# Optimization experiments

Hardware: AMD Instinct MI355X
Metric: run time of the kernel (lower is better)

Reference implementation:

```python
import jax, jax.numpy as jnp
import numpy as np

MUL = 1024
DIMS = [3, 5, 7, 9]          # irrep dims for l=1,2,3,4
BN_EPS = 1e-5                # e3nn BatchNorm eps
ACT_EPS = 1e-8               # numerical guard for norm-activation sqrt
INV_SQRT_MUL = 1.0 / np.sqrt(MUL)


def bn_act(f, w):
    """e3nn BatchNorm (training mode, component normalization, mean reduce)
    followed by NormActivation(sigmoid, normalize=True).
    f: [B, mul, d] one irrep block; w: [mul] affine batchnorm weight."""
    # norm-based batchnorm: second moment per multiplicity channel
    var = jnp.mean(jnp.mean(f * f, axis=-1), axis=0)            # [mul]
    f = f * ((var + BN_EPS) ** -0.5 * w)[None, :, None]
    # norm-gated sigmoid: out = f * sigmoid(||f||) / ||f||
    n = jnp.sqrt(jnp.sum(f * f, axis=-1, keepdims=True) + ACT_EPS)  # [B, mul, 1]
    return f * (jax.nn.sigmoid(n) / n)


def setup_inputs() -> dict:
    key = jax.random.key(0)
    k = jax.random.split(key, 4)
    B = 1024
    x = jax.random.normal(k[0], (B, 2, 3, 1), dtype=jnp.float32)
    w1 = jax.random.normal(k[1], (2, MUL), dtype=jnp.float32)
    W = jax.random.normal(k[2], (5, 4, MUL, MUL), dtype=jnp.float32)
    bn_w = jnp.ones((6, 4, MUL), dtype=jnp.float32)
    w_out = jax.random.normal(k[3], (MUL, 1), dtype=jnp.float32)
    return {"x": x, "w1": w1, "W": W, "bn_w": bn_w, "w_out": w_out}


def reference(x, w1, W, bn_w, w_out):
    B = x.shape[0]
    x = x.reshape(B, 2, 3)  # '2x1e'
    # block1: only the l=1 path exists; l=2,3,4 outputs are zero
    f1 = jnp.einsum('bui,uv->bvi', x, w1) * (1.0 / jnp.sqrt(2.0).astype(x.dtype))
    fields = [bn_act(f1, bn_w[0, 0])]
    for i, d in enumerate(DIMS[1:]):
        fields.append(bn_act(jnp.zeros((B, MUL, d), x.dtype), bn_w[0, i + 1]))
    # blocks 2..6: per-irrep block linear + norm batchnorm + norm activation
    for b in range(5):
        fields = [
            bn_act(jnp.einsum('bui,uv->bvi', f, W[b, i]) * INV_SQRT_MUL,
                   bn_w[b + 1, i])
            for i, f in enumerate(fields)
        ]
    # out linear: '1024x1e' -> '1x1e'
    out = jnp.einsum('bui,uv->bvi', fields[0], w_out) * INV_SQRT_MUL  # [B,1,3]
    return out.reshape(B, 3)
```

## Files before the change

### kernel.cpp

```cpp
#include <hip/hip_runtime.h>
#include <hip/hip_bf16.h>
#include <cstdint>
#include <cstddef>


typedef short    s16x8 __attribute__((ext_vector_type(8)));
typedef float    f32x4 __attribute__((ext_vector_type(4)));

#define PLANE 1048576

__device__ __forceinline__ unsigned short f2bf(float f) {
  unsigned u = __builtin_bit_cast(unsigned, f);
  u += 0x7FFFu + ((u >> 16) & 1u);
  return (unsigned short)(u >> 16);
}
__device__ __forceinline__ float bf2f(unsigned short h) {
  return __builtin_bit_cast(float, (unsigned)h << 16);
}

__device__ __forceinline__ size_t ablk(int row, int k) {
  return ((size_t)(row >> 6) << 17) + ((size_t)(k >> 5) << 12)
       + ((size_t)((row >> 4) & 3) << 10) + ((size_t)((k >> 3) & 3) << 8)
       + ((size_t)(row & 15) << 4) + ((size_t)(k & 7) << 1);
}

__device__ __forceinline__ void load_lds16(const void* g, void* l) {
  __builtin_amdgcn_global_load_lds(
      (const __attribute__((address_space(1))) unsigned int*)g,
      (__attribute__((address_space(3))) unsigned int*)l,
      16, 0, 0);
}

__global__ void convert_w(const float* __restrict__ W,
                          unsigned short* __restrict__ Wh,
                          unsigned short* __restrict__ Wl) {
  __shared__ float t[64][65];
  const int u0 = blockIdx.x * 64, v0 = blockIdx.y * 64;
  const float* Wb = W + (size_t)blockIdx.z * 4194304;
  char* Whb = (char*)(Wh + (size_t)blockIdx.z * PLANE);
  char* Wlb = (char*)(Wl + (size_t)blockIdx.z * PLANE);
  const int c = threadIdx.x & 63, r4 = threadIdx.x >> 6;
#pragma unroll
  for (int i = 0; i < 16; ++i) {
    const int r = i * 4 + r4;
    t[r][c] = Wb[(size_t)(u0 + r) * 1024 + v0 + c];
  }
  __syncthreads();
#pragma unroll
  for (int i = 0; i < 16; ++i) {
    const int r = i * 4 + r4;
    const float w = t[c][r] * 0.03125f;
    const unsigned short hi = f2bf(w);
    const size_t off = ablk(v0 + r, u0 + c);
    *(unsigned short*)(Whb + off) = hi;
    *(unsigned short*)(Wlb + off) = f2bf(w - bf2f(hi));
  }
}

__global__ void layer0_fused(const float* __restrict__ x, const float* __restrict__ w1,
                             float* __restrict__ pre, float* __restrict__ var) {
  const int v = blockIdx.x * 256 + threadIdx.x;
  const int b0 = blockIdx.y * 16;
  const float a0 = w1[v], a1 = w1[1024 + v];
  const float inv = 0.70710678118654752f;
  float ssq = 0.f;
#pragma unroll 4
  for (int bb = 0; bb < 16; ++bb) {
    const int b = b0 + bb;
    const float* xb = x + b * 6;
#pragma unroll
    for (int i = 0; i < 3; ++i) {
      const float f = (xb[i] * a0 + xb[3 + i] * a1) * inv;
      pre[(size_t)i * PLANE + (size_t)b * 1024 + v] = f;
      ssq += f * f;
    }
  }
  atomicAdd(&var[v], ssq);
}

__global__ void act_kernel(const float* __restrict__ pre, const float* __restrict__ var,
                           const float* __restrict__ bnw,
                           char* __restrict__ ah, char* __restrict__ al) {
  const int tid = threadIdx.x;
  const int b  = blockIdx.x * 16 + (tid & 15);
  const int v0 = blockIdx.y * 128 + (tid >> 4) * 8;
  float s[8];
#pragma unroll
  for (int j = 0; j < 8; ++j)
    s[j] = bnw[v0 + j] / sqrtf(var[v0 + j] * (1.0f / 3072.0f) + 1e-5f);
  float f[3][8];
#pragma unroll
  for (int i = 0; i < 3; ++i) {
    const float4 p0 = *(const float4*)&pre[(size_t)i * PLANE + (size_t)b * 1024 + v0];
    const float4 p1 = *(const float4*)&pre[(size_t)i * PLANE + (size_t)b * 1024 + v0 + 4];
    f[i][0] = p0.x * s[0]; f[i][1] = p0.y * s[1]; f[i][2] = p0.z * s[2]; f[i][3] = p0.w * s[3];
    f[i][4] = p1.x * s[4]; f[i][5] = p1.y * s[5]; f[i][6] = p1.z * s[6]; f[i][7] = p1.w * s[7];
  }
#pragma unroll
  for (int j = 0; j < 8; ++j) {
    const float n = sqrtf(f[0][j] * f[0][j] + f[1][j] * f[1][j] + f[2][j] * f[2][j] + 1e-8f);
    const float g = 1.0f / ((1.0f + expf(-n)) * n);
    f[0][j] *= g; f[1][j] *= g; f[2][j] *= g;
  }
#pragma unroll
  for (int i = 0; i < 3; ++i) {
    s16x8 hi, lo;
#pragma unroll
    for (int j = 0; j < 8; ++j) {
      const unsigned short h = f2bf(f[i][j]);
      hi[j] = (short)h;
      lo[j] = (short)f2bf(f[i][j] - bf2f(h));
    }
    const size_t off = ablk(i * 1024 + b, v0);
    *(s16x8*)(ah + off) = hi;
    *(s16x8*)(al + off) = lo;
  }
}

__global__ __launch_bounds__(256, 3) void gemm_fused(
    const char* __restrict__ Ah, const char* __restrict__ Al,
    const char* __restrict__ Bh, const char* __restrict__ Bl,
    float* __restrict__ C, float* __restrict__ var) {
  __shared__ unsigned short lds[3][4][4][4][16][8];
  const int tid = threadIdx.x;
  const int bid = blockIdx.x;
  const int xcd = bid & 7, q = bid >> 3;
  const int bm0 = (xcd * 6 + (q % 6)) * 64;
  const int bn0 = (q / 6) * 64;
  const int lane = tid & 63, wave = tid >> 6;
  const int wm = (wave >> 1) * 32, wn = (wave & 1) * 32;
  const int rsel = lane & 15, kcsel = lane >> 4;

  f32x4 acc[2][2] = {};

  const size_t abase = ((size_t)(bm0 >> 6) << 17) + (wave << 10) + (lane << 4);
  const size_t bbase = ((size_t)(bn0 >> 6) << 17) + (wave << 10) + (lane << 4);
  const char* g0 = Ah + abase;
  const char* g1 = Al + abase;
  const char* g2 = Bh + bbase;
  const char* g3 = Bl + bbase;

  auto stage = [&](int buf, int t) {
    const size_t kb = (size_t)t << 12;
    char* base = (char*)lds + buf * 16384 + (wave << 10);
    load_lds16(g0 + kb, base);
    load_lds16(g1 + kb, base + 4096);
    load_lds16(g2 + kb, base + 8192);
    load_lds16(g3 + kb, base + 12288);
  };

  const int fo = kcsel * 256 + rsel * 16;
  auto compute = [&](int buf) {
    const char* p = (const char*)lds + buf * 16384;
    s16x8 fah[2], fal[2], fbh[2], fbl[2];
#pragma unroll
    for (int m = 0; m < 2; ++m) {
      fah[m] = *(const s16x8*)(p         + ((wm >> 4) + m) * 1024 + fo);
      fal[m] = *(const s16x8*)(p + 4096  + ((wm >> 4) + m) * 1024 + fo);
    }
#pragma unroll
    for (int n = 0; n < 2; ++n) {
      fbh[n] = *(const s16x8*)(p + 8192  + ((wn >> 4) + n) * 1024 + fo);
      fbl[n] = *(const s16x8*)(p + 12288 + ((wn >> 4) + n) * 1024 + fo);
    }
#pragma unroll
    for (int m = 0; m < 2; ++m)
#pragma unroll
      for (int n = 0; n < 2; ++n) {
        acc[m][n] = __builtin_amdgcn_mfma_f32_16x16x32_bf16(fal[m], fbh[n], acc[m][n], 0, 0, 0);
        acc[m][n] = __builtin_amdgcn_mfma_f32_16x16x32_bf16(fah[m], fbl[n], acc[m][n], 0, 0, 0);
        acc[m][n] = __builtin_amdgcn_mfma_f32_16x16x32_bf16(fah[m], fbh[n], acc[m][n], 0, 0, 0);
      }
  };

  stage(0, 0);
  stage(1, 1);
  int cb = 0, sb = 2;
  for (int t = 0; t < 30; ++t) {
    stage(sb, t + 2);
    __builtin_amdgcn_sched_barrier(0);
    asm volatile("s_waitcnt vmcnt(8)" ::: "memory");
    __builtin_amdgcn_sched_barrier(0);
    __builtin_amdgcn_s_barrier();
    compute(cb);
    __builtin_amdgcn_sched_barrier(0);
    __builtin_amdgcn_s_barrier();
    sb = cb;
    cb = (cb == 2) ? 0 : cb + 1;
  }
  asm volatile("s_waitcnt vmcnt(4)" ::: "memory");
  __builtin_amdgcn_sched_barrier(0);
  __builtin_amdgcn_s_barrier();
  compute(0);
  asm volatile("s_waitcnt vmcnt(0)" ::: "memory");
  __builtin_amdgcn_sched_barrier(0);
  __builtin_amdgcn_s_barrier();
  compute(1);

  const int r0 = bm0 + wm + (kcsel << 2);
  const int c0 = bn0 + wn + rsel;
  float csq[2] = {0.f, 0.f};
#pragma unroll
  for (int m = 0; m < 2; ++m)
#pragma unroll
    for (int n = 0; n < 2; ++n)
#pragma unroll
      for (int j = 0; j < 4; ++j) {
        const float v = acc[m][n][j];
        C[(size_t)(r0 + m * 16 + j) * 1024 + c0 + n * 16] = v;
        csq[n] += v * v;
      }
#pragma unroll
  for (int n = 0; n < 2; ++n) {
    csq[n] += __shfl_xor(csq[n], 16);
    csq[n] += __shfl_xor(csq[n], 32);
  }
  if (kcsel == 0) {
#pragma unroll
    for (int n = 0; n < 2; ++n)
      atomicAdd(&var[c0 + n * 16], csq[n]);
  }
}

__global__ void final_kernel(const char* __restrict__ ah, const char* __restrict__ al,
                             const float* __restrict__ wout, float* __restrict__ out) {
  const int b = blockIdx.x, tid = threadIdx.x;
  __shared__ float red[3][4];
  float s[3] = {0.f, 0.f, 0.f};
  if (tid < 128) {
    const int v0 = tid * 8;
#pragma unroll
    for (int i = 0; i < 3; ++i) {
      const size_t off = ablk(i * 1024 + b, v0);
      const s16x8 hi = *(const s16x8*)(ah + off);
      const s16x8 lo = *(const s16x8*)(al + off);
#pragma unroll
      for (int j = 0; j < 8; ++j)
        s[i] += (bf2f((unsigned short)hi[j]) + bf2f((unsigned short)lo[j])) * wout[v0 + j];
    }
  }
#pragma unroll
  for (int i = 0; i < 3; ++i)
    for (int o = 32; o >= 1; o >>= 1) s[i] += __shfl_down(s[i], o);
  if ((tid & 63) == 0)
#pragma unroll
    for (int i = 0; i < 3; ++i) red[i][tid >> 6] = s[i];
  __syncthreads();
  if (tid < 3) {
    const float t = red[tid][0] + red[tid][1] + red[tid][2] + red[tid][3];
    out[b * 3 + tid] = t * 0.03125f;
  }
}

extern "C" void kernel_launch(void* const* d_in, const int* in_sizes, int n_in,
                              void* d_out, int out_size, void* d_ws, size_t ws_size,
                              hipStream_t stream) {
  const float* x    = (const float*)d_in[0];
  const float* w1   = (const float*)d_in[1];
  const float* W    = (const float*)d_in[2];
  const float* bnw  = (const float*)d_in[3];
  const float* wout = (const float*)d_in[4];
  float* out = (float*)d_out;

  char* ws = (char*)d_ws;
  float*          var = (float*)ws;
  float*          pre = (float*)(ws + 32768);
  char*           ah  = ws + 12615680;
  char*           al  = ws + 18907136;
  unsigned short* wh  = (unsigned short*)(ws + 25198592);
  unsigned short* wl  = (unsigned short*)(ws + 35684352);

  hipMemsetAsync(var, 0, 6 * 1024 * sizeof(float), stream);
  convert_w<<<dim3(16, 16, 5), 256, 0, stream>>>(W, wh, wl);
  layer0_fused<<<dim3(4, 64), 256, 0, stream>>>(x, w1, pre, var);
  act_kernel<<<dim3(64, 8), 256, 0, stream>>>(pre, var, bnw, ah, al);
  for (int b = 0; b < 5; ++b) {
    gemm_fused<<<768, 256, 0, stream>>>(
        ah, al, (const char*)(wh + (size_t)b * PLANE), (const char*)(wl + (size_t)b * PLANE),
        pre, var + (b + 1) * 1024);
    act_kernel<<<dim3(64, 8), 256, 0, stream>>>(pre, var + (b + 1) * 1024,
                                                bnw + (size_t)(b + 1) * 4096, ah, al);
  }
  final_kernel<<<1024, 256, 0, stream>>>(ah, al, wout, out);
}
```

Measured before the change: 207.6 us.

## Enlarge GEMM tiles to 128x128 with 512 threads and blocked C layout

The GEMM block tile grows from 64x64 with 256 threads to 128x128 with 512 threads and 8 waves, each wave computing 64x32. Pipelining drops from triple to double LDS buffering, and the grid shrinks from 768 to 192 blocks. C is written in a wave-blocked layout so each store is lane-contiguous, and the activation kernel reads it back through a matching index function. The aim is more operand reuse per LDS load and more coalesced C stores, at the cost of 192 blocks on a 256-CU part (under one wave of blocks), lower occupancy and shallower prefetch.

```diff
diff --git a/kernel.cpp b/kernel.cpp
--- a/kernel.cpp
+++ b/kernel.cpp
@@ -22,6 +22,17 @@
   return ((size_t)(row >> 6) << 17) + ((size_t)(k >> 5) << 12)
        + ((size_t)((row >> 4) & 3) << 10) + ((size_t)((k >> 3) & 3) << 8)
        + ((size_t)(row & 15) << 4) + ((size_t)(k & 7) << 1);
+}
+
+__device__ __forceinline__ size_t cblk(int r, int c) {
+  const int tM = r >> 7, tN = c >> 7;
+  const int rr = r & 127, cc = c & 127;
+  const int wave = ((rr >> 6) << 2) | (cc >> 5);
+  const int m = (rr >> 4) & 3, j = rr & 3;
+  const int n = (cc >> 4) & 1;
+  const int lane = (((rr >> 2) & 3) << 4) | (cc & 15);
+  return (((size_t)((tM * 8 + tN) * 8 + wave)) << 11)
+       + (size_t)(((((m << 1) | n) << 2) | j) << 6) + lane;
 }
 
 __device__ __forceinline__ void load_lds16(const void* g, void* l) {
@@ -78,7 +89,8 @@
   atomicAdd(&var[v], ssq);
 }
 
-__global__ void act_kernel(const float* __restrict__ pre, const float* __restrict__ var,
+template <bool BLK>
+__global__ void act_kernel(const float* __restrict__ Cin, const float* __restrict__ var,
                            const float* __restrict__ bnw,
                            char* __restrict__ ah, char* __restrict__ al) {
   const int tid = threadIdx.x;
@@ -91,8 +103,15 @@
   float f[3][8];
 #pragma unroll
   for (int i = 0; i < 3; ++i) {
-    const float4 p0 = *(const float4*)&pre[(size_t)i * PLANE + (size_t)b * 1024 + v0];
-    const float4 p1 = *(const float4*)&pre[(size_t)i * PLANE + (size_t)b * 1024 + v0 + 4];
+    float4 p0, p1;
+    if (BLK) {
+      const size_t ci = cblk(i * 1024 + b, v0);
+      p0 = *(const float4*)&Cin[ci];
+      p1 = *(const float4*)&Cin[ci + 4];
+    } else {
+      p0 = *(const float4*)&Cin[(size_t)i * PLANE + (size_t)b * 1024 + v0];
+      p1 = *(const float4*)&Cin[(size_t)i * PLANE + (size_t)b * 1024 + v0 + 4];
+    }
     f[i][0] = p0.x * s[0]; f[i][1] = p0.y * s[1]; f[i][2] = p0.z * s[2]; f[i][3] = p0.w * s[3];
     f[i][4] = p1.x * s[4]; f[i][5] = p1.y * s[5]; f[i][6] = p1.z * s[6]; f[i][7] = p1.w * s[7];
   }
@@ -117,54 +136,55 @@
   }
 }
 
-__global__ __launch_bounds__(256, 3) void gemm_fused(
+__global__ __launch_bounds__(512, 2) void gemm_fused(
     const char* __restrict__ Ah, const char* __restrict__ Al,
     const char* __restrict__ Bh, const char* __restrict__ Bl,
     float* __restrict__ C, float* __restrict__ var) {
-  __shared__ unsigned short lds[3][4][4][4][16][8];
+  __shared__ unsigned short lds[2][32][4][16][8];
   const int tid = threadIdx.x;
   const int bid = blockIdx.x;
   const int xcd = bid & 7, q = bid >> 3;
-  const int bm0 = (xcd * 6 + (q % 6)) * 64;
-  const int bn0 = (q / 6) * 64;
+  const int bm0 = (xcd * 3 + (q % 3)) * 128;
+  const int bn0 = (q / 3) * 128;
   const int lane = tid & 63, wave = tid >> 6;
-  const int wm = (wave >> 1) * 32, wn = (wave & 1) * 32;
+  const int wr = wave >> 2, wc = wave & 3;
   const int rsel = lane & 15, kcsel = lane >> 4;
 
-  f32x4 acc[2][2] = {};
-
-  const size_t abase = ((size_t)(bm0 >> 6) << 17) + (wave << 10) + (lane << 4);
-  const size_t bbase = ((size_t)(bn0 >> 6) << 17) + (wave << 10) + (lane << 4);
-  const char* g0 = Ah + abase;
-  const char* g1 = Al + abase;
-  const char* g2 = Bh + bbase;
-  const char* g3 = Bl + bbase;
+  f32x4 acc[4][2] = {};
+
+  const char* gsrc[4];
+#pragma unroll
+  for (int l = 0; l < 4; ++l) {
+    const int g = wave * 4 + l;
+    const int mat = g >> 3, rb = (g >> 2) & 1, wq = g & 3;
+    const char* base = (mat == 0) ? Ah : (mat == 1) ? Al : (mat == 2) ? Bh : Bl;
+    const int rowblk = ((mat < 2) ? (bm0 >> 6) : (bn0 >> 6)) + rb;
+    gsrc[l] = base + ((size_t)rowblk << 17) + (wq << 10) + (lane << 4);
+  }
 
   auto stage = [&](int buf, int t) {
-    const size_t kb = (size_t)t << 12;
-    char* base = (char*)lds + buf * 16384 + (wave << 10);
-    load_lds16(g0 + kb, base);
-    load_lds16(g1 + kb, base + 4096);
-    load_lds16(g2 + kb, base + 8192);
-    load_lds16(g3 + kb, base + 12288);
+    char* ld = (char*)lds + (buf << 15) + wave * 4096;
+#pragma unroll
+    for (int l = 0; l < 4; ++l)
+      load_lds16(gsrc[l] + ((size_t)t << 12), ld + l * 1024);
   };
 
   const int fo = kcsel * 256 + rsel * 16;
   auto compute = [&](int buf) {
-    const char* p = (const char*)lds + buf * 16384;
-    s16x8 fah[2], fal[2], fbh[2], fbl[2];
-#pragma unroll
-    for (int m = 0; m < 2; ++m) {
-      fah[m] = *(const s16x8*)(p         + ((wm >> 4) + m) * 1024 + fo);
-      fal[m] = *(const s16x8*)(p + 4096  + ((wm >> 4) + m) * 1024 + fo);
+    const char* p = (const char*)lds + (buf << 15);
+    s16x8 fah[4], fal[4], fbh[2], fbl[2];
+#pragma unroll
+    for (int m = 0; m < 4; ++m) {
+      fah[m] = *(const s16x8*)(p + ((wr * 4 + m) << 10) + fo);
+      fal[m] = *(const s16x8*)(p + ((8 + wr * 4 + m) << 10) + fo);
     }
 #pragma unroll
     for (int n = 0; n < 2; ++n) {
-      fbh[n] = *(const s16x8*)(p + 8192  + ((wn >> 4) + n) * 1024 + fo);
-      fbl[n] = *(const s16x8*)(p + 12288 + ((wn >> 4) + n) * 1024 + fo);
-    }
-#pragma unroll
-    for (int m = 0; m < 2; ++m)
+      fbh[n] = *(const s16x8*)(p + ((16 + wc * 2 + n) << 10) + fo);
+      fbl[n] = *(const s16x8*)(p + ((24 + wc * 2 + n) << 10) + fo);
+    }
+#pragma unroll
+    for (int m = 0; m < 4; ++m)
 #pragma unroll
       for (int n = 0; n < 2; ++n) {
         acc[m][n] = __builtin_amdgcn_mfma_f32_16x16x32_bf16(fal[m], fbh[n], acc[m][n], 0, 0, 0);
@@ -174,40 +194,33 @@
   };
 
   stage(0, 0);
-  stage(1, 1);
-  int cb = 0, sb = 2;
-  for (int t = 0; t < 30; ++t) {
-    stage(sb, t + 2);
+  for (int t = 0; t < 31; ++t) {
+    stage((t + 1) & 1, t + 1);
     __builtin_amdgcn_sched_barrier(0);
-    asm volatile("s_waitcnt vmcnt(8)" ::: "memory");
+    asm volatile("s_waitcnt vmcnt(4)" ::: "memory");
     __builtin_amdgcn_sched_barrier(0);
     __builtin_amdgcn_s_barrier();
-    compute(cb);
+    compute(t & 1);
     __builtin_amdgcn_sched_barrier(0);
     __builtin_amdgcn_s_barrier();
-    sb = cb;
-    cb = (cb == 2) ? 0 : cb + 1;
-  }
-  asm volatile("s_waitcnt vmcnt(4)" ::: "memory");
+  }
   __builtin_amdgcn_sched_barrier(0);
-  __builtin_amdgcn_s_barrier();
-  compute(0);
   asm volatile("s_waitcnt vmcnt(0)" ::: "memory");
   __builtin_amdgcn_sched_barrier(0);
   __builtin_amdgcn_s_barrier();
   compute(1);
 
-  const int r0 = bm0 + wm + (kcsel << 2);
-  const int c0 = bn0 + wn + rsel;
+  const int tM = bm0 >> 7, tN = bn0 >> 7;
+  float* cw = C + (((size_t)((tM * 8 + tN) * 8 + wave)) << 11) + lane;
   float csq[2] = {0.f, 0.f};
 #pragma unroll
-  for (int m = 0; m < 2; ++m)
+  for (int m = 0; m < 4; ++m)
 #pragma unroll
     for (int n = 0; n < 2; ++n)
 #pragma unroll
       for (int j = 0; j < 4; ++j) {
         const float v = acc[m][n][j];
-        C[(size_t)(r0 + m * 16 + j) * 1024 + c0 + n * 16] = v;
+        cw[((((m << 1) | n) << 2) | j) << 6] = v;
         csq[n] += v * v;
       }
 #pragma unroll
@@ -218,7 +231,7 @@
   if (kcsel == 0) {
 #pragma unroll
     for (int n = 0; n < 2; ++n)
-      atomicAdd(&var[c0 + n * 16], csq[n]);
+      atomicAdd(&var[bn0 + wc * 32 + n * 16 + rsel], csq[n]);
   }
 }
 
@@ -273,13 +286,13 @@
   hipMemsetAsync(var, 0, 6 * 1024 * sizeof(float), stream);
   convert_w<<<dim3(16, 16, 5), 256, 0, stream>>>(W, wh, wl);
   layer0_fused<<<dim3(4, 64), 256, 0, stream>>>(x, w1, pre, var);
-  act_kernel<<<dim3(64, 8), 256, 0, stream>>>(pre, var, bnw, ah, al);
+  act_kernel<false><<<dim3(64, 8), 256, 0, stream>>>(pre, var, bnw, ah, al);
   for (int b = 0; b < 5; ++b) {
-    gemm_fused<<<768, 256, 0, stream>>>(
+    gemm_fused<<<192, 512, 0, stream>>>(
         ah, al, (const char*)(wh + (size_t)b * PLANE), (const char*)(wl + (size_t)b * PLANE),
         pre, var + (b + 1) * 1024);
-    act_kernel<<<dim3(64, 8), 256, 0, stream>>>(pre, var + (b + 1) * 1024,
-                                                bnw + (size_t)(b + 1) * 4096, ah, al);
+    act_kernel<true><<<dim3(64, 8), 256, 0, stream>>>(pre, var + (b + 1) * 1024,
+                                                      bnw + (size_t)(b + 1) * 4096, ah, al);
   }
   final_kernel<<<1024, 256, 0, stream>>>(ah, al, wout, out);
 }
```

New measurement: 220.1 us. 6.0% more time.

## Replace LDS-staged 4-wave GEMM with single-wave register double-buffered GEMM

Applied to the files above, without the earlier changes.

The 64x64 output tile per block is now computed by one wave that loads A/B fragments directly from global memory into registers, double-buffered across k-steps. This drops the LDS staging and the block barriers. Each wave now holds a 4x4 accumulator tile and issues 48 MFMAs per k-step. The cost is four times fewer waves per block, higher register pressure, and no explicit wait control, so memory latency must be hidden by the register prefetch and by occupancy.

```diff
diff --git a/kernel.cpp b/kernel.cpp
--- a/kernel.cpp
+++ b/kernel.cpp
@@ -22,13 +22,6 @@
   return ((size_t)(row >> 6) << 17) + ((size_t)(k >> 5) << 12)
        + ((size_t)((row >> 4) & 3) << 10) + ((size_t)((k >> 3) & 3) << 8)
        + ((size_t)(row & 15) << 4) + ((size_t)(k & 7) << 1);
-}
-
-__device__ __forceinline__ void load_lds16(const void* g, void* l) {
-  __builtin_amdgcn_global_load_lds(
-      (const __attribute__((address_space(1))) unsigned int*)g,
-      (__attribute__((address_space(3))) unsigned int*)l,
-      16, 0, 0);
 }
 
 __global__ void convert_w(const float* __restrict__ W,
@@ -117,93 +110,70 @@
   }
 }
 
-__global__ __launch_bounds__(256, 3) void gemm_fused(
+#define LOADF(A_, B_, t_)                                                      \
+  {                                                                            \
+    const size_t kb_ = (size_t)(t_) << 12;                                     \
+    _Pragma("unroll")                                                          \
+    for (int m_ = 0; m_ < 4; ++m_) {                                           \
+      A_[m_]     = *(const s16x8*)(a_h + kb_ + (m_ << 10));                    \
+      A_[4 + m_] = *(const s16x8*)(a_l + kb_ + (m_ << 10));                    \
+      B_[m_]     = *(const s16x8*)(b_h + kb_ + (m_ << 10));                    \
+      B_[4 + m_] = *(const s16x8*)(b_l + kb_ + (m_ << 10));                    \
+    }                                                                          \
+  }
+#define COMPUTEF(A_, B_)                                                       \
+  {                                                                            \
+    _Pragma("unroll")                                                          \
+    for (int m_ = 0; m_ < 4; ++m_)                                             \
+      _Pragma("unroll")                                                        \
+      for (int n_ = 0; n_ < 4; ++n_) {                                         \
+        acc[m_][n_] = __builtin_amdgcn_mfma_f32_16x16x32_bf16(                 \
+            A_[4 + m_], B_[n_], acc[m_][n_], 0, 0, 0);                         \
+        acc[m_][n_] = __builtin_amdgcn_mfma_f32_16x16x32_bf16(                 \
+            A_[m_], B_[4 + n_], acc[m_][n_], 0, 0, 0);                         \
+        acc[m_][n_] = __builtin_amdgcn_mfma_f32_16x16x32_bf16(                 \
+            A_[m_], B_[n_], acc[m_][n_], 0, 0, 0);                             \
+      }                                                                        \
+  }
+
+__global__ __launch_bounds__(64, 2) void gemm_reg(
     const char* __restrict__ Ah, const char* __restrict__ Al,
     const char* __restrict__ Bh, const char* __restrict__ Bl,
     float* __restrict__ C, float* __restrict__ var) {
-  __shared__ unsigned short lds[3][4][4][4][16][8];
-  const int tid = threadIdx.x;
   const int bid = blockIdx.x;
   const int xcd = bid & 7, q = bid >> 3;
-  const int bm0 = (xcd * 6 + (q % 6)) * 64;
-  const int bn0 = (q / 6) * 64;
-  const int lane = tid & 63, wave = tid >> 6;
-  const int wm = (wave >> 1) * 32, wn = (wave & 1) * 32;
+  const int tm = xcd * 6 + (q % 6);
+  const int tn = q / 6;
+  const int lane = threadIdx.x;
   const int rsel = lane & 15, kcsel = lane >> 4;
 
-  f32x4 acc[2][2] = {};
-
-  const size_t abase = ((size_t)(bm0 >> 6) << 17) + (wave << 10) + (lane << 4);
-  const size_t bbase = ((size_t)(bn0 >> 6) << 17) + (wave << 10) + (lane << 4);
-  const char* g0 = Ah + abase;
-  const char* g1 = Al + abase;
-  const char* g2 = Bh + bbase;
-  const char* g3 = Bl + bbase;
-
-  auto stage = [&](int buf, int t) {
-    const size_t kb = (size_t)t << 12;
-    char* base = (char*)lds + buf * 16384 + (wave << 10);
-    load_lds16(g0 + kb, base);
-    load_lds16(g1 + kb, base + 4096);
-    load_lds16(g2 + kb, base + 8192);
-    load_lds16(g3 + kb, base + 12288);
-  };
-
-  const int fo = kcsel * 256 + rsel * 16;
-  auto compute = [&](int buf) {
-    const char* p = (const char*)lds + buf * 16384;
-    s16x8 fah[2], fal[2], fbh[2], fbl[2];
-#pragma unroll
-    for (int m = 0; m < 2; ++m) {
-      fah[m] = *(const s16x8*)(p         + ((wm >> 4) + m) * 1024 + fo);
-      fal[m] = *(const s16x8*)(p + 4096  + ((wm >> 4) + m) * 1024 + fo);
-    }
-#pragma unroll
-    for (int n = 0; n < 2; ++n) {
-      fbh[n] = *(const s16x8*)(p + 8192  + ((wn >> 4) + n) * 1024 + fo);
-      fbl[n] = *(const s16x8*)(p + 12288 + ((wn >> 4) + n) * 1024 + fo);
-    }
-#pragma unroll
-    for (int m = 0; m < 2; ++m)
-#pragma unroll
-      for (int n = 0; n < 2; ++n) {
-        acc[m][n] = __builtin_amdgcn_mfma_f32_16x16x32_bf16(fal[m], fbh[n], acc[m][n], 0, 0, 0);
-        acc[m][n] = __builtin_amdgcn_mfma_f32_16x16x32_bf16(fah[m], fbl[n], acc[m][n], 0, 0, 0);
-        acc[m][n] = __builtin_amdgcn_mfma_f32_16x16x32_bf16(fah[m], fbh[n], acc[m][n], 0, 0, 0);
-      }
-  };
-
-  stage(0, 0);
-  stage(1, 1);
-  int cb = 0, sb = 2;
-  for (int t = 0; t < 30; ++t) {
-    stage(sb, t + 2);
-    __builtin_amdgcn_sched_barrier(0);
-    asm volatile("s_waitcnt vmcnt(8)" ::: "memory");
-    __builtin_amdgcn_sched_barrier(0);
-    __builtin_amdgcn_s_barrier();
-    compute(cb);
-    __builtin_amdgcn_sched_barrier(0);
-    __builtin_amdgcn_s_barrier();
-    sb = cb;
-    cb = (cb == 2) ? 0 : cb + 1;
-  }
-  asm volatile("s_waitcnt vmcnt(4)" ::: "memory");
-  __builtin_amdgcn_sched_barrier(0);
-  __builtin_amdgcn_s_barrier();
-  compute(0);
-  asm volatile("s_waitcnt vmcnt(0)" ::: "memory");
-  __builtin_amdgcn_sched_barrier(0);
-  __builtin_amdgcn_s_barrier();
-  compute(1);
-
-  const int r0 = bm0 + wm + (kcsel << 2);
-  const int c0 = bn0 + wn + rsel;
-  float csq[2] = {0.f, 0.f};
-#pragma unroll
-  for (int m = 0; m < 2; ++m)
-#pragma unroll
-    for (int n = 0; n < 2; ++n)
+  const size_t la = (size_t)lane << 4;
+  const char* a_h = Ah + ((size_t)tm << 17) + la;
+  const char* a_l = Al + ((size_t)tm << 17) + la;
+  const char* b_h = Bh + ((size_t)tn << 17) + la;
+  const char* b_l = Bl + ((size_t)tn << 17) + la;
+
+  f32x4 acc[4][4] = {};
+  s16x8 A0[8], B0[8], A1[8], B1[8];
+
+  LOADF(A0, B0, 0);
+  LOADF(A1, B1, 1);
+  for (int t = 0; t < 30; t += 2) {
+    COMPUTEF(A0, B0);
+    LOADF(A0, B0, t + 2);
+    COMPUTEF(A1, B1);
+    LOADF(A1, B1, t + 3);
+  }
+  COMPUTEF(A0, B0);
+  COMPUTEF(A1, B1);
+
+  const int r0 = tm * 64 + (kcsel << 2);
+  const int c0 = tn * 64 + rsel;
+  float csq[4] = {0.f, 0.f, 0.f, 0.f};
+#pragma unroll
+  for (int m = 0; m < 4; ++m)
+#pragma unroll
+    for (int n = 0; n < 4; ++n)
 #pragma unroll
       for (int j = 0; j < 4; ++j) {
         const float v = acc[m][n][j];
@@ -211,13 +181,13 @@
         csq[n] += v * v;
       }
 #pragma unroll
-  for (int n = 0; n < 2; ++n) {
+  for (int n = 0; n < 4; ++n) {
     csq[n] += __shfl_xor(csq[n], 16);
     csq[n] += __shfl_xor(csq[n], 32);
   }
   if (kcsel == 0) {
 #pragma unroll
-    for (int n = 0; n < 2; ++n)
+    for (int n = 0; n < 4; ++n)
       atomicAdd(&var[c0 + n * 16], csq[n]);
   }
 }
@@ -275,7 +245,7 @@
   layer0_fused<<<dim3(4, 64), 256, 0, stream>>>(x, w1, pre, var);
   act_kernel<<<dim3(64, 8), 256, 0, stream>>>(pre, var, bnw, ah, al);
   for (int b = 0; b < 5; ++b) {
-    gemm_fused<<<768, 256, 0, stream>>>(
+    gemm_reg<<<768, 64, 0, stream>>>(
         ah, al, (const char*)(wh + (size_t)b * PLANE), (const char*)(wl + (size_t)b * PLANE),
         pre, var + (b + 1) * 1024);
     act_kernel<<<dim3(64, 8), 256, 0, stream>>>(pre, var + (b + 1) * 1024,
```

After: 205.8 us. Within noise of the previous version (-0.9%).
